# Kernel optimization log

Hardware: AMD Instinct MI355X
Metric: run time of the kernel (lower is better)

The kernel has to match this reference:

```python
import jax, jax.numpy as jnp
import numpy as np

N = 20000          # num proposals (nodes)
E = 320000         # num edges
IN = 4096          # roi feature dim
EMB = 200          # glove embed dim
HID = 512          # hidden dim
NH = 8             # heads (conv1)
HC = HID // NH     # 64 per-head channels
NCLS = 151         # VG object classes
NEG_SLOPE = 0.2    # PyG GATConv leaky_relu slope


def setup_inputs() -> dict:
    key = jax.random.key(0)
    ks = jax.random.split(key, 18)
    d_in1 = IN + EMB + 128  # 4424, conv1 input dim
    inp = {
        "roi_features": jax.random.normal(ks[0], (N, IN), jnp.float32),
        "box_info": jax.random.uniform(ks[1], (N, 9), jnp.float32),
        # embedding tables
        "emb1": jax.random.normal(ks[2], (NCLS, EMB), jnp.float32) * 0.02,
        "emb2": jax.random.normal(ks[3], (NCLS, EMB), jnp.float32) * 0.02,
        # bbox MLP 9 -> 32 -> 128
        "bw1": jax.random.normal(ks[4], (9, 32), jnp.float32) / np.sqrt(9),
        "bb1": jnp.zeros((32,), jnp.float32),
        "bw2": jax.random.normal(ks[5], (32, 128), jnp.float32) / np.sqrt(32),
        "bb2": jnp.zeros((128,), jnp.float32),
        # GATConv1: d_in1 -> 8 heads x 64, concat
        "W1": jax.random.normal(ks[6], (d_in1, NH * HC), jnp.float32) / np.sqrt(d_in1),
        "a_src1": jax.random.normal(ks[7], (NH, HC), jnp.float32) * 0.1,
        "a_dst1": jax.random.normal(ks[8], (NH, HC), jnp.float32) * 0.1,
        "bias1": jnp.zeros((NH * HC,), jnp.float32),
        # GATConv2: 512 -> 512, 1 head, concat=False
        "W2": jax.random.normal(ks[9], (HID, HID), jnp.float32) / np.sqrt(HID),
        "a_src2": jax.random.normal(ks[10], (1, HID), jnp.float32) * 0.1,
        "a_dst2": jax.random.normal(ks[11], (1, HID), jnp.float32) * 0.1,
        "bias2": jnp.zeros((HID,), jnp.float32),
        # int inputs
        "obj_labels": jax.random.randint(ks[12], (N,), 0, NCLS, jnp.int32),
        "edge_index": jax.random.randint(ks[13], (2, E), 0, N, jnp.int32),
    }
    return inp


def _segment_softmax(logits, seg, n):
    # logits: [E, H]; softmax over edges sharing the same destination seg id
    m = jax.ops.segment_max(logits, seg, num_segments=n)
    e = jnp.exp(logits - m[seg])
    s = jax.ops.segment_sum(e, seg, num_segments=n)
    return e / (s[seg] + 1e-16)


def _gat_conv(x, src, dst, W, a_src, a_dst, bias, concat):
    # PyG GATConv (self-loops already included in src/dst); dropout off (eval)
    n = x.shape[0]
    H, C = a_src.shape
    h = (x @ W).reshape(n, H, C)                      # [N, H, C]
    al_s = jnp.einsum('nhc,hc->nh', h, a_src)         # [N, H]
    al_d = jnp.einsum('nhc,hc->nh', h, a_dst)
    logits = jax.nn.leaky_relu(al_s[src] + al_d[dst], NEG_SLOPE)  # [E, H]
    alpha = _segment_softmax(logits, dst, n)          # [E, H]
    out = jax.ops.segment_sum(alpha[:, :, None] * h[src], dst, num_segments=n)
    out = out.reshape(n, H * C) if concat else out.mean(axis=1)
    return out + bias


def reference(roi_features, box_info, emb1, emb2, bw1, bb1, bw2, bb2,
              W1, a_src1, a_dst1, bias1, W2, a_src2, a_dst2, bias2,
              obj_labels, edge_index):
    n = roi_features.shape[0]
    # predcls mode: GT labels -> embedding lookup
    obj_embed = emb1[obj_labels]                              # [N, 200]
    pos = jax.nn.relu(box_info @ bw1 + bb1)
    pos = jax.nn.relu(pos @ bw2 + bb2)                        # [N, 128]
    x = jnp.concatenate([roi_features, obj_embed, pos], -1)  # [N, 4424]

    # add self-loops (PyG GATConv default)
    ar = jnp.arange(n, dtype=edge_index.dtype)
    src = jnp.concatenate([edge_index[0], ar])
    dst = jnp.concatenate([edge_index[1], ar])

    edge_f1 = jax.nn.elu(_gat_conv(x, src, dst, W1, a_src1, a_dst1, bias1, True))
    obj_feats = _gat_conv(edge_f1, src, dst, W2, a_src2, a_dst2, bias2, False)

    obj_dists = jax.nn.one_hot(obj_labels, NCLS, dtype=jnp.float32)
    edge_pre_rep = jnp.concatenate([roi_features, obj_feats, emb2[obj_labels]], -1)
    return obj_dists, obj_labels, edge_pre_rep
```

## Files before the change

### kernel.cpp

```cpp
#include <hip/hip_runtime.h>
#include <hip/hip_bf16.h>

#define NNODES 20000
#define NEDGES 320000
#define ETOT   (NEDGES + NNODES)
#define KPAD1  4448
#define MPAD   20096
#define NCLS   151
#define EPRW   4808
#define OUT_LAB_OFF  3020000L
#define OUT_EPR_OFF  3040000L
#define NSLOPE 0.2f

typedef __attribute__((ext_vector_type(8))) short bf16x8;
typedef __attribute__((ext_vector_type(4))) float f32x4;

__device__ __forceinline__ short f2bf(float v) {
  union { __hip_bfloat16 b; short s; } u;
  u.b = __float2bfloat16(v);
  return u.s;
}

__device__ __forceinline__ float bf2f(short s) {
  union { float f; unsigned u; } x;
  x.u = ((unsigned)(unsigned short)s) << 16;
  return x.f;
}

__device__ __forceinline__ void gld16(const short* g, short* l) {
  __builtin_amdgcn_global_load_lds(
      (const __attribute__((address_space(1))) unsigned int*)g,
      (__attribute__((address_space(3))) unsigned int*)l, 16, 0, 0);
}

__global__ __launch_bounds__(256) void build_x_kernel(
    const float* __restrict__ roi, const float* __restrict__ box,
    const float* __restrict__ emb1, const float* __restrict__ emb2,
    const float* __restrict__ bw1, const float* __restrict__ bb1,
    const float* __restrict__ bw2, const float* __restrict__ bb2,
    const int* __restrict__ labels,
    short* __restrict__ x, float* __restrict__ dout) {
  const int n = blockIdx.x;
  const int tid = threadIdx.x;
  __shared__ float hid[32];
  __shared__ float bx[9];
  if (tid < 9) bx[tid] = box[n * 9 + tid];
  __syncthreads();
  if (tid < 32) {
    float a = bb1[tid];
#pragma unroll
    for (int i = 0; i < 9; ++i) a += bx[i] * bw1[i * 32 + tid];
    hid[tid] = a > 0.f ? a : 0.f;
  }
  __syncthreads();
  const long xrow = (long)n * KPAD1;
  if (tid < 128) {
    float a = bb2[tid];
#pragma unroll
    for (int i = 0; i < 32; ++i) a += hid[i] * bw2[i * 128 + tid];
    a = a > 0.f ? a : 0.f;
    x[xrow + 4296 + tid] = f2bf(a);
  }
  if (tid >= 128 && tid < 152) x[xrow + 4424 + (tid - 128)] = 0;
  const int lab = labels[n];
  float* epr = dout + OUT_EPR_OFF + (long)n * EPRW;
#pragma unroll
  for (int j = tid * 4; j < 4096; j += 1024) {
    const float4 v = *(const float4*)&roi[(long)n * 4096 + j];
    *(float4*)&epr[j] = v;
    short4 b;
    b.x = f2bf(v.x); b.y = f2bf(v.y); b.z = f2bf(v.z); b.w = f2bf(v.w);
    *(short4*)&x[xrow + j] = b;
  }
  if (tid < 50) {
    const int j = tid * 4;
    const float4 e1 = *(const float4*)&emb1[lab * 200 + j];
    short4 b;
    b.x = f2bf(e1.x); b.y = f2bf(e1.y); b.z = f2bf(e1.z); b.w = f2bf(e1.w);
    *(short4*)&x[xrow + 4096 + j] = b;
    *(float4*)&epr[4608 + j] = *(const float4*)&emb2[lab * 200 + j];
  }
  for (int j = tid; j < NCLS; j += 256)
    dout[(long)n * NCLS + j] = (j == lab) ? 1.f : 0.f;
  if (tid == 0) dout[OUT_LAB_OFF + n] = (float)lab;
}

__global__ void pad_zero_kernel(short* __restrict__ x, short* __restrict__ ef1,
                                int* __restrict__ deg) {
  const int t = blockIdx.x * 256 + threadIdx.x;
  if (t < 96 * KPAD1) x[(long)NNODES * KPAD1 + t] = 0;
  if (t < 96 * 512)   ef1[(long)NNODES * 512 + t] = 0;
  if (t < NNODES)     deg[t] = 0;
}

__global__ __launch_bounds__(256) void transpose_w_kernel(
    const float* __restrict__ W, short* __restrict__ WT, int K, int Kpad, int Ncols) {
  __shared__ float tile[32][33];
  const int n0 = blockIdx.x * 32;
  const int k0 = blockIdx.y * 32;
  const int tx = threadIdx.x;
  const int ty = threadIdx.y;
#pragma unroll
  for (int i = ty; i < 32; i += 8) {
    const int k = k0 + i;
    tile[i][tx] = (k < K) ? W[(long)k * Ncols + (n0 + tx)] : 0.f;
  }
  __syncthreads();
#pragma unroll
  for (int i = ty; i < 32; i += 8) {
    WT[(long)(n0 + i) * Kpad + (k0 + tx)] = f2bf(tile[tx][i]);
  }
}

__global__ __launch_bounds__(256) void gemm_bt(const short* __restrict__ A,
                                               const short* __restrict__ BT,
                                               short* __restrict__ C,
                                               int Kpad, int Ncols) {
  __shared__ short As[4096];
  __shared__ short Bs[4096];
  const int tid = threadIdx.x;
  const int lane = tid & 63;
  const int w = tid >> 6;
  const int wr = w >> 1, wc = w & 1;
  const long bm = (long)blockIdx.x * 128;
  const long bn = (long)blockIdx.y * 128;

  f32x4 acc[4][4] = {};

  const short* gA0 = A + (bm + w * 32 + (lane >> 2)) * (long)Kpad + (lane & 3) * 8;
  const short* gA1 = gA0 + 16L * Kpad;
  const short* gB0 = BT + (bn + w * 32 + (lane >> 2)) * (long)Kpad + (lane & 3) * 8;
  const short* gB1 = gB0 + 16L * Kpad;
  short* lA0 = &As[w * 1024];
  short* lA1 = &As[w * 1024 + 512];
  short* lB0 = &Bs[w * 1024];
  short* lB1 = &Bs[w * 1024 + 512];

  const int ar = (wr * 64 + (lane & 15)) * 32 + (lane >> 4) * 8;
  const int br = (wc * 64 + (lane & 15)) * 32 + (lane >> 4) * 8;

  for (int k0 = 0; k0 < Kpad; k0 += 32) {
    gld16(gA0, lA0); gld16(gA1, lA1);
    gld16(gB0, lB0); gld16(gB1, lB1);
    gA0 += 32; gA1 += 32; gB0 += 32; gB1 += 32;
    asm volatile("s_waitcnt vmcnt(0)" ::: "memory");
    __syncthreads();
    bf16x8 a[4], b[4];
#pragma unroll
    for (int mi = 0; mi < 4; ++mi) a[mi] = *(const bf16x8*)&As[ar + mi * 512];
#pragma unroll
    for (int ni = 0; ni < 4; ++ni) b[ni] = *(const bf16x8*)&Bs[br + ni * 512];
#pragma unroll
    for (int mi = 0; mi < 4; ++mi)
#pragma unroll
      for (int ni = 0; ni < 4; ++ni)
        acc[mi][ni] = __builtin_amdgcn_mfma_f32_16x16x32_bf16(a[mi], b[ni], acc[mi][ni], 0, 0, 0);
    __syncthreads();
  }

#pragma unroll
  for (int mi = 0; mi < 4; ++mi) {
#pragma unroll
    for (int ni = 0; ni < 4; ++ni) {
      const long row0 = bm + wr * 64 + mi * 16 + (lane >> 4) * 4;
      const long col  = bn + wc * 64 + ni * 16 + (lane & 15);
#pragma unroll
      for (int r = 0; r < 4; ++r)
        C[(row0 + r) * (long)Ncols + col] = f2bf(acc[mi][ni][r]);
    }
  }
}

__global__ __launch_bounds__(256) void alsd1_kernel(const short* __restrict__ h,
    const float* __restrict__ a_src, const float* __restrict__ a_dst,
    float* __restrict__ als, float* __restrict__ ald) {
  const int g = (blockIdx.x * 256 + threadIdx.x) >> 6;
  const int lane = threadIdx.x & 63;
  if (g >= NNODES * 8) return;
  const int node = g >> 3, hh = g & 7;
  const float v = bf2f(h[(long)node * 512 + hh * 64 + lane]);
  float s = v * a_src[hh * 64 + lane];
  float d = v * a_dst[hh * 64 + lane];
#pragma unroll
  for (int o = 32; o > 0; o >>= 1) { s += __shfl_xor(s, o); d += __shfl_xor(d, o); }
  if (lane == 0) { als[g] = s; ald[g] = d; }
}

__global__ __launch_bounds__(256) void alsd2_kernel(const short* __restrict__ h,
    const float* __restrict__ a_src, const float* __restrict__ a_dst,
    float* __restrict__ als, float* __restrict__ ald) {
  const int g = (blockIdx.x * 256 + threadIdx.x) >> 6;
  const int lane = threadIdx.x & 63;
  if (g >= NNODES) return;
  float s = 0.f, d = 0.f;
#pragma unroll
  for (int j = 0; j < 8; ++j) {
    const int c = j * 64 + lane;
    const float v = bf2f(h[(long)g * 512 + c]);
    s += v * a_src[c];
    d += v * a_dst[c];
  }
#pragma unroll
  for (int o = 32; o > 0; o >>= 1) { s += __shfl_xor(s, o); d += __shfl_xor(d, o); }
  if (lane == 0) { als[g] = s; ald[g] = d; }
}

__global__ void deg_count_kernel(const int* __restrict__ ei, int* __restrict__ deg) {
  const int e = blockIdx.x * 256 + threadIdx.x;
  if (e >= ETOT) return;
  const int d = (e < NEDGES) ? ei[NEDGES + e] : (e - NEDGES);
  atomicAdd(&deg[d], 1);
}

__global__ __launch_bounds__(256) void scan_kernel(const int* __restrict__ deg,
                                                   int* __restrict__ off,
                                                   int* __restrict__ cur) {
  __shared__ int part[256];
  const int tid = threadIdx.x;
  const int chunk = (NNODES + 255) / 256;
  int start = tid * chunk;
  int end = start + chunk; if (end > NNODES) end = NNODES;
  int s = 0;
  for (int i = start; i < end; ++i) s += deg[i];
  part[tid] = s;
  __syncthreads();
  for (int d = 1; d < 256; d <<= 1) {
    const int v = (tid >= d) ? part[tid - d] : 0;
    __syncthreads();
    part[tid] += v;
    __syncthreads();
  }
  int base = part[tid] - s;
  for (int i = start; i < end; ++i) { off[i] = base; cur[i] = base; base += deg[i]; }
}

__global__ void csr_fill_kernel(const int* __restrict__ ei, int* __restrict__ cur,
                                int* __restrict__ csrs) {
  const int e = blockIdx.x * 256 + threadIdx.x;
  if (e >= ETOT) return;
  const int s = (e < NEDGES) ? ei[e] : (e - NEDGES);
  const int d = (e < NEDGES) ? ei[NEDGES + e] : (e - NEDGES);
  csrs[atomicAdd(&cur[d], 1)] = s;
}

__global__ __launch_bounds__(128) void gather1_kernel(const int* __restrict__ off,
    const int* __restrict__ csrs,
    const float* __restrict__ als, const float* __restrict__ ald,
    const short* __restrict__ h1, const float* __restrict__ bias,
    short* __restrict__ ef1) {
  const int dn = blockIdx.x;
  const int tid = threadIdx.x;
  const int c0 = tid * 4;
  const int h = c0 >> 6;
  const int beg = off[dn];
  const int end = (dn == NNODES - 1) ? ETOT : off[dn + 1];
  const float ad = ald[dn * 8 + h];
  float sum = 0.f, a0 = 0.f, a1 = 0.f, a2 = 0.f, a3 = 0.f;
  for (int i = beg; i < end; ++i) {
    const int s = csrs[i];
    float l = als[s * 8 + h] + ad;
    l = l > 0.f ? l : NSLOPE * l;
    const float wgt = expf(l);
    sum += wgt;
    const short4 hv = *(const short4*)&h1[(long)s * 512 + c0];
    a0 += wgt * bf2f(hv.x);
    a1 += wgt * bf2f(hv.y);
    a2 += wgt * bf2f(hv.z);
    a3 += wgt * bf2f(hv.w);
  }
  const float inv = 1.f / (sum + 1e-16f);
  float r0 = a0 * inv + bias[c0];
  float r1 = a1 * inv + bias[c0 + 1];
  float r2 = a2 * inv + bias[c0 + 2];
  float r3 = a3 * inv + bias[c0 + 3];
  r0 = r0 > 0.f ? r0 : expm1f(r0);
  r1 = r1 > 0.f ? r1 : expm1f(r1);
  r2 = r2 > 0.f ? r2 : expm1f(r2);
  r3 = r3 > 0.f ? r3 : expm1f(r3);
  short4 out;
  out.x = f2bf(r0); out.y = f2bf(r1); out.z = f2bf(r2); out.w = f2bf(r3);
  *(short4*)&ef1[(long)dn * 512 + c0] = out;
}

__global__ __launch_bounds__(128) void gather2_kernel(const int* __restrict__ off,
    const int* __restrict__ csrs,
    const float* __restrict__ als, const float* __restrict__ ald,
    const short* __restrict__ h2, const float* __restrict__ bias,
    float* __restrict__ dout) {
  const int dn = blockIdx.x;
  const int tid = threadIdx.x;
  const int c0 = tid * 4;
  const int beg = off[dn];
  const int end = (dn == NNODES - 1) ? ETOT : off[dn + 1];
  const float ad = ald[dn];
  float sum = 0.f, a0 = 0.f, a1 = 0.f, a2 = 0.f, a3 = 0.f;
  for (int i = beg; i < end; ++i) {
    const int s = csrs[i];
    float l = als[s] + ad;
    l = l > 0.f ? l : NSLOPE * l;
    const float wgt = expf(l);
    sum += wgt;
    const short4 hv = *(const short4*)&h2[(long)s * 512 + c0];
    a0 += wgt * bf2f(hv.x);
    a1 += wgt * bf2f(hv.y);
    a2 += wgt * bf2f(hv.z);
    a3 += wgt * bf2f(hv.w);
  }
  const float inv = 1.f / (sum + 1e-16f);
  float4 out;
  out.x = a0 * inv + bias[c0];
  out.y = a1 * inv + bias[c0 + 1];
  out.z = a2 * inv + bias[c0 + 2];
  out.w = a3 * inv + bias[c0 + 3];
  float* epr = dout + OUT_EPR_OFF + (long)dn * EPRW + 4096;
  *(float4*)&epr[c0] = out;
}

extern "C" void kernel_launch(void* const* d_in, const int* in_sizes, int n_in,
                              void* d_out, int out_size, void* d_ws, size_t ws_size,
                              hipStream_t stream) {
  const float* roi  = (const float*)d_in[0];
  const float* box  = (const float*)d_in[1];
  const float* emb1 = (const float*)d_in[2];
  const float* emb2 = (const float*)d_in[3];
  const float* bw1  = (const float*)d_in[4];
  const float* bb1  = (const float*)d_in[5];
  const float* bw2  = (const float*)d_in[6];
  const float* bb2  = (const float*)d_in[7];
  const float* W1   = (const float*)d_in[8];
  const float* as1  = (const float*)d_in[9];
  const float* ad1  = (const float*)d_in[10];
  const float* b1   = (const float*)d_in[11];
  const float* W2   = (const float*)d_in[12];
  const float* as2  = (const float*)d_in[13];
  const float* ad2  = (const float*)d_in[14];
  const float* b2   = (const float*)d_in[15];
  const int* labels = (const int*)d_in[16];
  const int* ei     = (const int*)d_in[17];
  float* dout = (float*)d_out;

  char* wsb = (char*)d_ws;
  size_t o = 0;
  auto alloc = [&](size_t bytes) -> void* {
    void* p = wsb + o;
    o += (bytes + 255) & ~(size_t)255;
    return p;
  };
  short* x    = (short*)alloc((size_t)MPAD * KPAD1 * 2);
  short* w1t  = (short*)alloc((size_t)512 * KPAD1 * 2);
  short* h1   = (short*)alloc((size_t)MPAD * 512 * 2);
  short* ef1  = (short*)alloc((size_t)MPAD * 512 * 2);
  short* w2t  = (short*)alloc((size_t)512 * 512 * 2);
  short* h2   = (short*)alloc((size_t)MPAD * 512 * 2);
  float* als1 = (float*)alloc((size_t)NNODES * 8 * 4);
  float* ald1 = (float*)alloc((size_t)NNODES * 8 * 4);
  float* als2 = (float*)alloc((size_t)NNODES * 4);
  float* ald2 = (float*)alloc((size_t)NNODES * 4);
  int*   deg  = (int*)alloc((size_t)NNODES * 4);
  int*   offs = (int*)alloc((size_t)NNODES * 4);
  int*   cur  = (int*)alloc((size_t)NNODES * 4);
  int*   csrs = (int*)alloc((size_t)ETOT * 4);

  const int EB = (ETOT + 255) / 256;

  hipLaunchKernelGGL(build_x_kernel, dim3(NNODES), dim3(256), 0, stream,
                     roi, box, emb1, emb2, bw1, bb1, bw2, bb2, labels, x, dout);
  hipLaunchKernelGGL(pad_zero_kernel, dim3((96 * KPAD1 + 255) / 256), dim3(256), 0, stream,
                     x, ef1, deg);
  hipLaunchKernelGGL(transpose_w_kernel, dim3(512 / 32, KPAD1 / 32), dim3(32, 8), 0, stream,
                     W1, w1t, 4424, KPAD1, 512);
  hipLaunchKernelGGL(transpose_w_kernel, dim3(512 / 32, 512 / 32), dim3(32, 8), 0, stream,
                     W2, w2t, 512, 512, 512);
  hipLaunchKernelGGL(deg_count_kernel, dim3(EB), dim3(256), 0, stream, ei, deg);
  hipLaunchKernelGGL(scan_kernel, dim3(1), dim3(256), 0, stream, deg, offs, cur);
  hipLaunchKernelGGL(csr_fill_kernel, dim3(EB), dim3(256), 0, stream, ei, cur, csrs);
  hipLaunchKernelGGL(gemm_bt, dim3(MPAD / 128, 4), dim3(256), 0, stream,
                     x, w1t, h1, KPAD1, 512);
  hipLaunchKernelGGL(alsd1_kernel, dim3(NNODES * 8 * 64 / 256), dim3(256), 0, stream,
                     h1, as1, ad1, als1, ald1);
  hipLaunchKernelGGL(gather1_kernel, dim3(NNODES), dim3(128), 0, stream,
                     offs, csrs, als1, ald1, h1, b1, ef1);
  hipLaunchKernelGGL(gemm_bt, dim3(MPAD / 128, 4), dim3(256), 0, stream,
                     ef1, w2t, h2, 512, 512);
  hipLaunchKernelGGL(alsd2_kernel, dim3(NNODES * 64 / 256), dim3(256), 0, stream,
                     h2, as2, ad2, als2, ald2);
  hipLaunchKernelGGL(gather2_kernel, dim3(NNODES), dim3(128), 0, stream,
                     offs, csrs, als2, ald2, h2, b2, dout);
}
```

Baseline: 598.7 us.

## Fuse attention logit dot products into GEMM epilogue and widen gather per wave

Computes the per-node source and destination attention logits inside the GEMM epilogue from the fp32 accumulators, using shuffle reductions and atomic adds. This removes the separate alsd kernels and their re-read of h. The logit buffers are now zero-initialised in the init kernel. The gather kernels also switch to one wave per destination node with 8-wide bf16 loads, packing four nodes per block. The trade-offs are atomics in the epilogue and a logit now computed from unrounded fp32 values rather than bf16.

```diff
diff --git a/kernel.cpp b/kernel.cpp
--- a/kernel.cpp
+++ b/kernel.cpp
@@ -85,12 +85,16 @@
   if (tid == 0) dout[OUT_LAB_OFF + n] = (float)lab;
 }
 
-__global__ void pad_zero_kernel(short* __restrict__ x, short* __restrict__ ef1,
-                                int* __restrict__ deg) {
+__global__ void misc_init_kernel(short* __restrict__ x, short* __restrict__ ef1,
+                                 int* __restrict__ deg,
+                                 float* __restrict__ als1, float* __restrict__ ald1,
+                                 float* __restrict__ als2, float* __restrict__ ald2) {
   const int t = blockIdx.x * 256 + threadIdx.x;
   if (t < 96 * KPAD1) x[(long)NNODES * KPAD1 + t] = 0;
   if (t < 96 * 512)   ef1[(long)NNODES * 512 + t] = 0;
   if (t < NNODES)     deg[t] = 0;
+  if (t < MPAD * 8)   { als1[t] = 0.f; ald1[t] = 0.f; }
+  if (t < MPAD)       { als2[t] = 0.f; ald2[t] = 0.f; }
 }
 
 __global__ __launch_bounds__(256) void transpose_w_kernel(
@@ -115,7 +119,11 @@
 __global__ __launch_bounds__(256) void gemm_bt(const short* __restrict__ A,
                                                const short* __restrict__ BT,
                                                short* __restrict__ C,
-                                               int Kpad, int Ncols) {
+                                               const float* __restrict__ aS,
+                                               const float* __restrict__ aD,
+                                               float* __restrict__ als,
+                                               float* __restrict__ ald,
+                                               int Kpad, int Ncols, int H) {
   __shared__ short As[4096];
   __shared__ short Bs[4096];
   const int tid = threadIdx.x;
@@ -169,40 +177,38 @@
         C[(row0 + r) * (long)Ncols + col] = f2bf(acc[mi][ni][r]);
     }
   }
-}
-
-__global__ __launch_bounds__(256) void alsd1_kernel(const short* __restrict__ h,
-    const float* __restrict__ a_src, const float* __restrict__ a_dst,
-    float* __restrict__ als, float* __restrict__ ald) {
-  const int g = (blockIdx.x * 256 + threadIdx.x) >> 6;
-  const int lane = threadIdx.x & 63;
-  if (g >= NNODES * 8) return;
-  const int node = g >> 3, hh = g & 7;
-  const float v = bf2f(h[(long)node * 512 + hh * 64 + lane]);
-  float s = v * a_src[hh * 64 + lane];
-  float d = v * a_dst[hh * 64 + lane];
-#pragma unroll
-  for (int o = 32; o > 0; o >>= 1) { s += __shfl_xor(s, o); d += __shfl_xor(d, o); }
-  if (lane == 0) { als[g] = s; ald[g] = d; }
-}
-
-__global__ __launch_bounds__(256) void alsd2_kernel(const short* __restrict__ h,
-    const float* __restrict__ a_src, const float* __restrict__ a_dst,
-    float* __restrict__ als, float* __restrict__ ald) {
-  const int g = (blockIdx.x * 256 + threadIdx.x) >> 6;
-  const int lane = threadIdx.x & 63;
-  if (g >= NNODES) return;
-  float s = 0.f, d = 0.f;
-#pragma unroll
-  for (int j = 0; j < 8; ++j) {
-    const int c = j * 64 + lane;
-    const float v = bf2f(h[(long)g * 512 + c]);
-    s += v * a_src[c];
-    d += v * a_dst[c];
-  }
-#pragma unroll
-  for (int o = 32; o > 0; o >>= 1) { s += __shfl_xor(s, o); d += __shfl_xor(d, o); }
-  if (lane == 0) { als[g] = s; ald[g] = d; }
+
+  const int colb = (int)bn + wc * 64 + (lane & 15);
+  float asv[4], adv[4];
+#pragma unroll
+  for (int ni = 0; ni < 4; ++ni) {
+    asv[ni] = aS[colb + ni * 16];
+    adv[ni] = aD[colb + ni * 16];
+  }
+  const int head = (H == 8) ? (((int)bn >> 6) + wc) : 0;
+#pragma unroll
+  for (int mi = 0; mi < 4; ++mi) {
+#pragma unroll
+    for (int r = 0; r < 4; ++r) {
+      float s = 0.f, d = 0.f;
+#pragma unroll
+      for (int ni = 0; ni < 4; ++ni) {
+        const float v = acc[mi][ni][r];
+        s += v * asv[ni];
+        d += v * adv[ni];
+      }
+#pragma unroll
+      for (int o = 1; o < 16; o <<= 1) {
+        s += __shfl_xor(s, o);
+        d += __shfl_xor(d, o);
+      }
+      if ((lane & 15) == 0) {
+        const long row = bm + wr * 64 + mi * 16 + (lane >> 4) * 4 + r;
+        atomicAdd(&als[row * H + head], s);
+        atomicAdd(&ald[row * H + head], d);
+      }
+    }
+  }
 }
 
 __global__ void deg_count_kernel(const int* __restrict__ ei, int* __restrict__ deg) {
@@ -243,77 +249,77 @@
   csrs[atomicAdd(&cur[d], 1)] = s;
 }
 
-__global__ __launch_bounds__(128) void gather1_kernel(const int* __restrict__ off,
+__global__ __launch_bounds__(256) void gather1_kernel(const int* __restrict__ off,
     const int* __restrict__ csrs,
     const float* __restrict__ als, const float* __restrict__ ald,
     const short* __restrict__ h1, const float* __restrict__ bias,
     short* __restrict__ ef1) {
-  const int dn = blockIdx.x;
-  const int tid = threadIdx.x;
-  const int c0 = tid * 4;
-  const int h = c0 >> 6;
+  const int dn = blockIdx.x * 4 + (threadIdx.x >> 6);
+  const int lane = threadIdx.x & 63;
+  const int c0 = lane * 8;
+  const int head = lane >> 3;
   const int beg = off[dn];
   const int end = (dn == NNODES - 1) ? ETOT : off[dn + 1];
-  const float ad = ald[dn * 8 + h];
-  float sum = 0.f, a0 = 0.f, a1 = 0.f, a2 = 0.f, a3 = 0.f;
+  const float ad = ald[dn * 8 + head];
+  float sum = 0.f;
+  float acc[8] = {};
   for (int i = beg; i < end; ++i) {
     const int s = csrs[i];
-    float l = als[s * 8 + h] + ad;
+    float l = als[s * 8 + head] + ad;
     l = l > 0.f ? l : NSLOPE * l;
     const float wgt = expf(l);
     sum += wgt;
-    const short4 hv = *(const short4*)&h1[(long)s * 512 + c0];
-    a0 += wgt * bf2f(hv.x);
-    a1 += wgt * bf2f(hv.y);
-    a2 += wgt * bf2f(hv.z);
-    a3 += wgt * bf2f(hv.w);
+    const bf16x8 hv = *(const bf16x8*)&h1[(long)s * 512 + c0];
+#pragma unroll
+    for (int j = 0; j < 8; ++j) acc[j] += wgt * bf2f(hv[j]);
   }
   const float inv = 1.f / (sum + 1e-16f);
-  float r0 = a0 * inv + bias[c0];
-  float r1 = a1 * inv + bias[c0 + 1];
-  float r2 = a2 * inv + bias[c0 + 2];
-  float r3 = a3 * inv + bias[c0 + 3];
-  r0 = r0 > 0.f ? r0 : expm1f(r0);
-  r1 = r1 > 0.f ? r1 : expm1f(r1);
-  r2 = r2 > 0.f ? r2 : expm1f(r2);
-  r3 = r3 > 0.f ? r3 : expm1f(r3);
-  short4 out;
-  out.x = f2bf(r0); out.y = f2bf(r1); out.z = f2bf(r2); out.w = f2bf(r3);
-  *(short4*)&ef1[(long)dn * 512 + c0] = out;
-}
-
-__global__ __launch_bounds__(128) void gather2_kernel(const int* __restrict__ off,
+  bf16x8 outv;
+#pragma unroll
+  for (int j = 0; j < 8; ++j) {
+    float r = acc[j] * inv + bias[c0 + j];
+    r = r > 0.f ? r : expm1f(r);
+    outv[j] = f2bf(r);
+  }
+  *(bf16x8*)&ef1[(long)dn * 512 + c0] = outv;
+}
+
+__global__ __launch_bounds__(256) void gather2_kernel(const int* __restrict__ off,
     const int* __restrict__ csrs,
     const float* __restrict__ als, const float* __restrict__ ald,
     const short* __restrict__ h2, const float* __restrict__ bias,
     float* __restrict__ dout) {
-  const int dn = blockIdx.x;
-  const int tid = threadIdx.x;
-  const int c0 = tid * 4;
+  const int dn = blockIdx.x * 4 + (threadIdx.x >> 6);
+  const int lane = threadIdx.x & 63;
+  const int c0 = lane * 8;
   const int beg = off[dn];
   const int end = (dn == NNODES - 1) ? ETOT : off[dn + 1];
   const float ad = ald[dn];
-  float sum = 0.f, a0 = 0.f, a1 = 0.f, a2 = 0.f, a3 = 0.f;
+  float sum = 0.f;
+  float acc[8] = {};
   for (int i = beg; i < end; ++i) {
     const int s = csrs[i];
     float l = als[s] + ad;
     l = l > 0.f ? l : NSLOPE * l;
     const float wgt = expf(l);
     sum += wgt;
-    const short4 hv = *(const short4*)&h2[(long)s * 512 + c0];
-    a0 += wgt * bf2f(hv.x);
-    a1 += wgt * bf2f(hv.y);
-    a2 += wgt * bf2f(hv.z);
-    a3 += wgt * bf2f(hv.w);
+    const bf16x8 hv = *(const bf16x8*)&h2[(long)s * 512 + c0];
+#pragma unroll
+    for (int j = 0; j < 8; ++j) acc[j] += wgt * bf2f(hv[j]);
   }
   const float inv = 1.f / (sum + 1e-16f);
-  float4 out;
-  out.x = a0 * inv + bias[c0];
-  out.y = a1 * inv + bias[c0 + 1];
-  out.z = a2 * inv + bias[c0 + 2];
-  out.w = a3 * inv + bias[c0 + 3];
   float* epr = dout + OUT_EPR_OFF + (long)dn * EPRW + 4096;
-  *(float4*)&epr[c0] = out;
+  float4 o0, o1;
+  o0.x = acc[0] * inv + bias[c0 + 0];
+  o0.y = acc[1] * inv + bias[c0 + 1];
+  o0.z = acc[2] * inv + bias[c0 + 2];
+  o0.w = acc[3] * inv + bias[c0 + 3];
+  o1.x = acc[4] * inv + bias[c0 + 4];
+  o1.y = acc[5] * inv + bias[c0 + 5];
+  o1.z = acc[6] * inv + bias[c0 + 6];
+  o1.w = acc[7] * inv + bias[c0 + 7];
+  *(float4*)&epr[c0]     = o0;
+  *(float4*)&epr[c0 + 4] = o1;
 }
 
 extern "C" void kernel_launch(void* const* d_in, const int* in_sizes, int n_in,
@@ -352,10 +358,10 @@
   short* ef1  = (short*)alloc((size_t)MPAD * 512 * 2);
   short* w2t  = (short*)alloc((size_t)512 * 512 * 2);
   short* h2   = (short*)alloc((size_t)MPAD * 512 * 2);
-  float* als1 = (float*)alloc((size_t)NNODES * 8 * 4);
-  float* ald1 = (float*)alloc((size_t)NNODES * 8 * 4);
-  float* als2 = (float*)alloc((size_t)NNODES * 4);
-  float* ald2 = (float*)alloc((size_t)NNODES * 4);
+  float* als1 = (float*)alloc((size_t)MPAD * 8 * 4);
+  float* ald1 = (float*)alloc((size_t)MPAD * 8 * 4);
+  float* als2 = (float*)alloc((size_t)MPAD * 4);
+  float* ald2 = (float*)alloc((size_t)MPAD * 4);
   int*   deg  = (int*)alloc((size_t)NNODES * 4);
   int*   offs = (int*)alloc((size_t)NNODES * 4);
   int*   cur  = (int*)alloc((size_t)NNODES * 4);
@@ -365,8 +371,8 @@
 
   hipLaunchKernelGGL(build_x_kernel, dim3(NNODES), dim3(256), 0, stream,
                      roi, box, emb1, emb2, bw1, bb1, bw2, bb2, labels, x, dout);
-  hipLaunchKernelGGL(pad_zero_kernel, dim3((96 * KPAD1 + 255) / 256), dim3(256), 0, stream,
-                     x, ef1, deg);
+  hipLaunchKernelGGL(misc_init_kernel, dim3((96 * KPAD1 + 255) / 256), dim3(256), 0, stream,
+                     x, ef1, deg, als1, ald1, als2, ald2);
   hipLaunchKernelGGL(transpose_w_kernel, dim3(512 / 32, KPAD1 / 32), dim3(32, 8), 0, stream,
                      W1, w1t, 4424, KPAD1, 512);
   hipLaunchKernelGGL(transpose_w_kernel, dim3(512 / 32, 512 / 32), dim3(32, 8), 0, stream,
@@ -375,15 +381,11 @@
   hipLaunchKernelGGL(scan_kernel, dim3(1), dim3(256), 0, stream, deg, offs, cur);
   hipLaunchKernelGGL(csr_fill_kernel, dim3(EB), dim3(256), 0, stream, ei, cur, csrs);
   hipLaunchKernelGGL(gemm_bt, dim3(MPAD / 128, 4), dim3(256), 0, stream,
-                     x, w1t, h1, KPAD1, 512);
-  hipLaunchKernelGGL(alsd1_kernel, dim3(NNODES * 8 * 64 / 256), dim3(256), 0, stream,
-                     h1, as1, ad1, als1, ald1);
-  hipLaunchKernelGGL(gather1_kernel, dim3(NNODES), dim3(128), 0, stream,
+                     x, w1t, h1, as1, ad1, als1, ald1, KPAD1, 512, 8);
+  hipLaunchKernelGGL(gather1_kernel, dim3(NNODES / 4), dim3(256), 0, stream,
                      offs, csrs, als1, ald1, h1, b1, ef1);
   hipLaunchKernelGGL(gemm_bt, dim3(MPAD / 128, 4), dim3(256), 0, stream,
-                     ef1, w2t, h2, 512, 512);
-  hipLaunchKernelGGL(alsd2_kernel, dim3(NNODES * 64 / 256), dim3(256), 0, stream,
-                     h2, as2, ad2, als2, ald2);
-  hipLaunchKernelGGL(gather2_kernel, dim3(NNODES), dim3(128), 0, stream,
+                     ef1, w2t, h2, as2, ad2, als2, ald2, 512, 512, 1);
+  hipLaunchKernelGGL(gather2_kernel, dim3(NNODES / 4), dim3(256), 0, stream,
                      offs, csrs, als2, ald2, h2, b2, dout);
 }
```

Measured after the change: 593.0 us. Within noise of the previous version (-1.0%).
